# Kernel tuning notes

Hardware: AMD Instinct MI355X
Metric: run time of the kernel (lower is better)

Reference implementation:

```python
import jax, jax.numpy as jnp
import numpy as np

EPS = 1e-5

def _ln(x, g, b):
    m = x.mean(-1, keepdims=True)
    v = ((x - m) ** 2).mean(-1, keepdims=True)
    return (x - m) * jax.lax.rsqrt(v + EPS) * g + b

def _dwconv3d(x, w, stride):
    # x: [N, C, T, H, W], w: [C, 1, kt, kh, kw], depthwise (groups=C), pad = k//2 = 1
    return jax.lax.conv_general_dilated(
        x, w, window_strides=stride, padding=[(1, 1), (1, 1), (1, 1)],
        dimension_numbers=('NCDHW', 'OIDHW', 'NCDHW'), feature_group_count=x.shape[1])

def _pool_heads(t4, w, g, b, stride, thw):
    # t4: [B, nH, 1+L, hd] with cls token at index 0
    B, nH, _, hd = t4.shape
    T, H, W = thw
    cls_tok, body = t4[:, :, :1, :], t4[:, :, 1:, :]
    x = body.reshape(B * nH, T, H, W, hd).transpose(0, 4, 1, 2, 3)  # [B*nH, hd, T, H, W]
    x = _dwconv3d(x, w, stride)
    Tn, Hn, Wn = x.shape[2], x.shape[3], x.shape[4]
    x = x.reshape(B, nH, hd, Tn * Hn * Wn).transpose(0, 1, 3, 2)  # [B, nH, L', hd]
    x = jnp.concatenate([cls_tok, x], axis=2)
    return _ln(x, g, b), (Tn, Hn, Wn)

def _maxpool_skip(x, thw, kernel=(1, 3, 3), stride=(1, 2, 2), pad=((0, 0), (1, 1), (1, 1))):
    # x: [B, 1+L, C]
    B, _, C = x.shape
    T, H, W = thw
    cls_tok, body = x[:, :1, :], x[:, 1:, :]
    y = body.reshape(B, T, H, W, C).transpose(0, 4, 1, 2, 3)  # [B, C, T, H, W]
    y = jax.lax.reduce_window(
        y, -jnp.inf, jax.lax.max,
        window_dimensions=(1, 1) + kernel, window_strides=(1, 1) + stride,
        padding=((0, 0), (0, 0)) + pad)
    Lp = y.shape[2] * y.shape[3] * y.shape[4]
    y = y.reshape(B, C, Lp).transpose(0, 2, 1)
    return jnp.concatenate([cls_tok, y], axis=1)

def setup_inputs() -> dict:
    key = jax.random.key(0)
    ks = jax.random.split(key, 12)
    B, T, H, W, D, NH, HD, DOUT, HID = 16, 8, 28, 28, 192, 2, 96, 384, 768
    N = 1 + T * H * W
    s = 0.02
    return {
        'x': jax.random.normal(ks[0], (B, N, D), jnp.float32),
        'ln1_g': jnp.ones((D,), jnp.float32), 'ln1_b': jnp.zeros((D,), jnp.float32),
        'qkv_w': jax.random.normal(ks[1], (D, 3 * D), jnp.float32) * s,
        'qkv_b': jnp.zeros((3 * D,), jnp.float32),
        'pq_w': jax.random.normal(ks[2], (HD, 1, 3, 3, 3), jnp.float32) * s,
        'pk_w': jax.random.normal(ks[3], (HD, 1, 3, 3, 3), jnp.float32) * s,
        'pv_w': jax.random.normal(ks[4], (HD, 1, 3, 3, 3), jnp.float32) * s,
        'nq_g': jnp.ones((HD,), jnp.float32), 'nq_b': jnp.zeros((HD,), jnp.float32),
        'nk_g': jnp.ones((HD,), jnp.float32), 'nk_b': jnp.zeros((HD,), jnp.float32),
        'nv_g': jnp.ones((HD,), jnp.float32), 'nv_b': jnp.zeros((HD,), jnp.float32),
        'proj_w': jax.random.normal(ks[5], (D, D), jnp.float32) * s,
        'proj_b': jnp.zeros((D,), jnp.float32),
        'ln2_g': jnp.ones((D,), jnp.float32), 'ln2_b': jnp.zeros((D,), jnp.float32),
        'fc1_w': jax.random.normal(ks[6], (D, HID), jnp.float32) * s,
        'fc1_b': jnp.zeros((HID,), jnp.float32),
        'fc2_w': jax.random.normal(ks[7], (HID, DOUT), jnp.float32) * s,
        'fc2_b': jnp.zeros((DOUT,), jnp.float32),
        'projd_w': jax.random.normal(ks[8], (D, DOUT), jnp.float32) * s,
        'projd_b': jnp.zeros((DOUT,), jnp.float32),
        't': T, 'h': H, 'w': W,
    }

def reference(x, ln1_g, ln1_b, qkv_w, qkv_b, pq_w, pk_w, pv_w,
              nq_g, nq_b, nk_g, nk_b, nv_g, nv_b, proj_w, proj_b,
              ln2_g, ln2_b, fc1_w, fc1_b, fc2_w, fc2_b, projd_w, projd_b,
              t, h, w):
    thw = (t, h, w)
    B, N, C = x.shape
    NH = 2
    hd = C // NH
    scale = hd ** -0.5
    stride_q = (1, 2, 2)
    stride_kv = (1, 2, 2)

    # --- attention branch ---
    xn = _ln(x, ln1_g, ln1_b)
    qkv = (xn @ qkv_w + qkv_b).reshape(B, N, 3, NH, hd).transpose(2, 0, 3, 1, 4)
    q, k, v = qkv[0], qkv[1], qkv[2]  # [B, NH, N, hd]
    q, out_shape = _pool_heads(q, pq_w, nq_g, nq_b, stride_q, thw)
    k, _ = _pool_heads(k, pk_w, nk_g, nk_b, stride_kv, thw)
    v, _ = _pool_heads(v, pv_w, nv_g, nv_b, stride_kv, thw)
    attn = jax.nn.softmax(jnp.einsum('bhqd,bhkd->bhqk', q, k) * scale, axis=-1)
    o = jnp.einsum('bhqk,bhkd->bhqd', attn, v)  # [B, NH, Lq, hd]
    Lq = o.shape[2]
    o = o.transpose(0, 2, 1, 3).reshape(B, Lq, C)
    x_block = o @ proj_w + proj_b

    # --- residual skip with max-pool (kernel_skip=(1,3,3) from stride_q=(1,2,2)) ---
    x_res = _maxpool_skip(x, thw)
    x1 = x_res + x_block

    # --- MLP branch (dim != dim_out -> proj on norm2 output) ---
    xn2 = _ln(x1, ln2_g, ln2_b)
    hmid = jax.nn.gelu(xn2 @ fc1_w + fc1_b, approximate=False)
    x_mlp = hmid @ fc2_w + fc2_b
    x2 = (xn2 @ projd_w + projd_b) + x_mlp
    return x2
```

## Files before the change

kernel.cpp:

```cpp
#include <hip/hip_runtime.h>
#include <hip/hip_bf16.h>
#include <type_traits>

#define BB   16
#define N0   6273
#define NQ   1569
#define C3   576
#define HID  768
#define DOUT 384
#define M1   (BB*N0)
#define M2   (BB*NQ)

typedef __attribute__((ext_vector_type(8))) short  s16x8;
typedef __attribute__((ext_vector_type(8))) __bf16 bf16x8;
typedef __attribute__((ext_vector_type(4))) float  f32x4;

static __device__ __forceinline__ float bf2f(unsigned short u) {
  return __uint_as_float(((unsigned)u) << 16);
}
static __device__ __forceinline__ unsigned short f2bf(float f) {
  unsigned x = __float_as_uint(f);
  x += 0x7fffu + ((x >> 16) & 1u);
  return (unsigned short)(x >> 16);
}
static __device__ __forceinline__ unsigned pk2(float a, float b) {
  return (unsigned)f2bf(a) | ((unsigned)f2bf(b) << 16);
}

__global__ __launch_bounds__(256) void ln_rows_bf16_kernel(
    const float* __restrict__ in, const float* __restrict__ g,
    const float* __restrict__ bta, unsigned short* __restrict__ out,
    int rows, int ldc) {
  int row = blockIdx.x * 4 + (threadIdx.x >> 6);
  int lane = threadIdx.x & 63;
  if (row >= rows) return;
  const float* p = in + (size_t)row * 192;
  float v0 = p[lane], v1 = p[lane + 64], v2 = p[lane + 128];
  float s = v0 + v1 + v2;
  float q = v0 * v0 + v1 * v1 + v2 * v2;
  #pragma unroll
  for (int m = 32; m; m >>= 1) { s += __shfl_xor(s, m, 64); q += __shfl_xor(q, m, 64); }
  float mean = s * (1.f / 192.f);
  float var  = q * (1.f / 192.f) - mean * mean;
  float rstd = rsqrtf(var + 1e-5f);
  unsigned short* po = out + (size_t)row * ldc;
  po[lane]       = f2bf((v0 - mean) * rstd * g[lane]       + bta[lane]);
  po[lane + 64]  = f2bf((v1 - mean) * rstd * g[lane + 64]  + bta[lane + 64]);
  po[lane + 128] = f2bf((v2 - mean) * rstd * g[lane + 128] + bta[lane + 128]);
}

__global__ __launch_bounds__(256) void wtrans_kernel(
    const float* __restrict__ in, unsigned short* __restrict__ out, int K, int N) {
  int idx = blockIdx.x * 256 + threadIdx.x;
  if (idx >= K * N) return;
  int n = idx / K, k = idx - n * K;
  out[idx] = f2bf(in[k * N + n]);
}

__global__ __launch_bounds__(256) void wcomb_kernel(
    const float* __restrict__ fc2w, const float* __restrict__ projdw,
    const float* __restrict__ fc2b, const float* __restrict__ projdb,
    unsigned short* __restrict__ wT, float* __restrict__ bc) {
  int idx = blockIdx.x * 256 + threadIdx.x;
  if (idx < 384 * 960) {
    int n = idx / 960, k = idx - n * 960;
    float v = (k < 768) ? fc2w[k * 384 + n] : projdw[(k - 768) * 384 + n];
    wT[idx] = f2bf(v);
  }
  if (idx < 384) bc[idx] = fc2b[idx] + projdb[idx];
}

template <int ACT, int BETA, typename TC>
__global__ __launch_bounds__(256) void gemm_mfma_kernel(
    const unsigned short* __restrict__ A, const unsigned short* __restrict__ BT,
    const float* __restrict__ bias, TC* __restrict__ C,
    int M, int N, int K, int lda, int ldc) {
  __shared__ alignas(16) unsigned short As[128 * 64];
  __shared__ alignas(16) unsigned short Bs[64 * 64];
  const int tid = threadIdx.x;
  const int lane = tid & 63, wid = tid >> 6;
  const int lo = lane & 15, hi = lane >> 4;
  const int bm = blockIdx.y * 128;
  const int bn = blockIdx.x * 64;
  const int s_row = tid >> 3;
  const int s_cb  = tid & 7;
  const int wrow  = wid * 32;
  char* asb = (char*)As;
  char* bsb = (char*)Bs;
  f32x4 acc[2][4];
  #pragma unroll
  for (int mi = 0; mi < 2; ++mi)
    #pragma unroll
    for (int nj = 0; nj < 4; ++nj) {
      acc[mi][nj][0] = 0.f; acc[mi][nj][1] = 0.f;
      acc[mi][nj][2] = 0.f; acc[mi][nj][3] = 0.f;
    }
  for (int k0 = 0; k0 < K; k0 += 64) {
    uint4 av[4], bv[2];
    #pragma unroll
    for (int i = 0; i < 4; ++i) {
      int row = s_row + 32 * i;
      int rg = bm + row; if (rg > M - 1) rg = M - 1;
      av[i] = *(const uint4*)(A + (size_t)rg * lda + k0 + s_cb * 8);
    }
    #pragma unroll
    for (int i = 0; i < 2; ++i) {
      int col = s_row + 32 * i;
      bv[i] = *(const uint4*)(BT + (size_t)(bn + col) * K + k0 + s_cb * 8);
    }
    if (k0) __syncthreads();
    #pragma unroll
    for (int i = 0; i < 4; ++i) {
      int row = s_row + 32 * i;
      *(uint4*)(asb + row * 128 + ((s_cb ^ (row & 7)) << 4)) = av[i];
    }
    #pragma unroll
    for (int i = 0; i < 2; ++i) {
      int col = s_row + 32 * i;
      *(uint4*)(bsb + col * 128 + ((s_cb ^ (col & 7)) << 4)) = bv[i];
    }
    __syncthreads();
    #pragma unroll
    for (int ks = 0; ks < 2; ++ks) {
      s16x8 af[2], bf[4];
      #pragma unroll
      for (int mi = 0; mi < 2; ++mi) {
        int row = wrow + mi * 16 + lo;
        af[mi] = *(const s16x8*)(asb + row * 128 + (((ks * 4 + hi) ^ (row & 7)) << 4));
      }
      #pragma unroll
      for (int nj = 0; nj < 4; ++nj) {
        int col = nj * 16 + lo;
        bf[nj] = *(const s16x8*)(bsb + col * 128 + (((ks * 4 + hi) ^ (col & 7)) << 4));
      }
      #pragma unroll
      for (int mi = 0; mi < 2; ++mi)
        #pragma unroll
        for (int nj = 0; nj < 4; ++nj)
          acc[mi][nj] = __builtin_amdgcn_mfma_f32_16x16x32_bf16(
              (bf16x8)af[mi], (bf16x8)bf[nj], acc[mi][nj], 0, 0, 0);
    }
  }
  #pragma unroll
  for (int nj = 0; nj < 4; ++nj) {
    float bsv = bias[bn + nj * 16 + lo];
    #pragma unroll
    for (int mi = 0; mi < 2; ++mi) {
      int rowb = bm + wrow + mi * 16 + hi * 4;
      #pragma unroll
      for (int r = 0; r < 4; ++r) {
        int row = rowb + r;
        if (row >= M) continue;
        float v = acc[mi][nj][r] + bsv;
        if (ACT == 1) v = 0.5f * v * (1.f + erff(v * 0.70710678118654752f));
        size_t oi = (size_t)row * ldc + bn + nj * 16 + lo;
        if constexpr (BETA != 0) {
          if constexpr (std::is_same<TC, float>::value) v += C[oi];
          else v += bf2f(C[oi]);
        }
        if constexpr (std::is_same<TC, float>::value) C[oi] = v;
        else C[oi] = f2bf(v);
      }
    }
  }
}

__global__ __launch_bounds__(128) void pool_ln_kernel(
    const unsigned short* __restrict__ qkv, const float* __restrict__ w,
    const float* __restrict__ g, const float* __restrict__ bb,
    unsigned short* __restrict__ outp, int cidx, float oscale) {
  const int bid = blockIdx.x;
  const int l  = bid % NQ;
  const int bh = bid / NQ;
  const int h  = bh & 1;
  const int b  = bh >> 1;
  const int d  = threadIdx.x;
  __shared__ float red[128];
  __shared__ float stats[2];
  float val = 0.f;
  if (d < 96) {
    const unsigned short* base = qkv + (size_t)b * N0 * C3 + cidx * 192 + h * 96 + d;
    if (l == 0) {
      val = bf2f(base[0]);
    } else {
      int lp = l - 1;
      int to = lp / 196;
      int rem = lp - to * 196;
      int ho = rem / 14;
      int wo = rem - ho * 14;
      const float* wd = w + d * 27;
      #pragma unroll
      for (int kt = 0; kt < 3; ++kt) {
        int it = to + kt - 1;
        if ((unsigned)it >= 8u) continue;
        #pragma unroll
        for (int kh = 0; kh < 3; ++kh) {
          int ih = 2 * ho + kh - 1;
          if ((unsigned)ih >= 28u) continue;
          #pragma unroll
          for (int kw = 0; kw < 3; ++kw) {
            int iw = 2 * wo + kw - 1;
            if ((unsigned)iw >= 28u) continue;
            int n = 1 + (it * 28 + ih) * 28 + iw;
            val += wd[(kt * 3 + kh) * 3 + kw] * bf2f(base[(size_t)n * C3]);
          }
        }
      }
    }
  }
  red[d] = (d < 96) ? val : 0.f;
  __syncthreads();
  for (int s = 64; s > 0; s >>= 1) { if (d < s) red[d] += red[d + s]; __syncthreads(); }
  if (d == 0) stats[0] = red[0] * (1.f / 96.f);
  __syncthreads();
  float mean = stats[0];
  float dv = (d < 96) ? (val - mean) : 0.f;
  red[d] = dv * dv;
  __syncthreads();
  for (int s = 64; s > 0; s >>= 1) { if (d < s) red[d] += red[d + s]; __syncthreads(); }
  if (d == 0) stats[1] = rsqrtf(red[0] * (1.f / 96.f) + 1e-5f);
  __syncthreads();
  if (d < 96)
    outp[((size_t)bh * NQ + l) * 96 + d] =
        f2bf(((val - mean) * stats[1] * g[d] + bb[d]) * oscale);
}

__global__ __launch_bounds__(256) void attn_mfma_kernel(
    const unsigned short* __restrict__ qb, const unsigned short* __restrict__ kb,
    const unsigned short* __restrict__ vb, unsigned short* __restrict__ o) {
  __shared__ alignas(16) unsigned short Ks[32][104];
  __shared__ alignas(16) unsigned short Vt[96 * 32];
  const int tid  = threadIdx.x;
  const int lane = tid & 63;
  const int wid  = tid >> 6;
  const int lo = lane & 15, hi = lane >> 4;
  const int bh = blockIdx.y;
  const int b = bh >> 1, h = bh & 1;
  const int q0 = blockIdx.x * 64 + wid * 16;
  const int qg = q0 + lo;

  const unsigned short* qbase = qb + (size_t)bh * NQ * 96;
  const unsigned short* kbase = kb + (size_t)bh * NQ * 96;
  const unsigned short* vbase = vb + (size_t)bh * NQ * 96;
  char* vtb = (char*)Vt;

  s16x8 qf[3];
  if (qg < NQ) {
    const unsigned short* qrow = qbase + (size_t)qg * 96 + hi * 8;
    qf[0] = *(const s16x8*)(qrow);
    qf[1] = *(const s16x8*)(qrow + 32);
    qf[2] = *(const s16x8*)(qrow + 64);
  } else {
    #pragma unroll
    for (int j = 0; j < 8; ++j) { qf[0][j] = 0; qf[1][j] = 0; qf[2][j] = 0; }
  }

  f32x4 ot[6];
  #pragma unroll
  for (int t = 0; t < 6; ++t) { ot[t][0] = 0.f; ot[t][1] = 0.f; ot[t][2] = 0.f; ot[t][3] = 0.f; }
  float m = -1e30f, lsum = 0.f;

  for (int c = 0; c < (NQ + 31) / 32; ++c) {
    const int k0 = c * 32;
    #pragma unroll
    for (int j = 0; j < 6; ++j) {
      int u = tid + 256 * j;
      int kr = u / 48, c2 = u - kr * 48;
      unsigned val = 0;
      if (k0 + kr < NQ)
        val = *(const unsigned*)(kbase + (size_t)(k0 + kr) * 96 + c2 * 2);
      *(unsigned*)(&Ks[kr][c2 * 2]) = val;
    }
    #pragma unroll
    for (int j = 0; j < 6; ++j) {
      int u = tid + 256 * j;
      int kr = u / 48, c2 = u - kr * 48;
      unsigned val = 0;
      if (k0 + kr < NQ)
        val = *(const unsigned*)(vbase + (size_t)(k0 + kr) * 96 + c2 * 2);
      int d0 = c2 * 2, d1 = d0 + 1;
      int o0 = (d0 * 64 + kr * 2) ^ ((d0 & 7) << 4);
      int o1 = (d1 * 64 + kr * 2) ^ ((d1 & 7) << 4);
      *(unsigned short*)(vtb + o0) = (unsigned short)(val & 0xffffu);
      *(unsigned short*)(vtb + o1) = (unsigned short)(val >> 16);
    }
    __syncthreads();
    f32x4 st0, st1;
    st0[0]=st0[1]=st0[2]=st0[3]=0.f;
    st1[0]=st1[1]=st1[2]=st1[3]=0.f;
    #pragma unroll
    for (int cc = 0; cc < 3; ++cc) {
      s16x8 kf0 = *(const s16x8*)(&Ks[lo][cc * 32 + hi * 8]);
      s16x8 kf1 = *(const s16x8*)(&Ks[16 + lo][cc * 32 + hi * 8]);
      st0 = __builtin_amdgcn_mfma_f32_16x16x32_bf16((bf16x8)kf0, (bf16x8)qf[cc], st0, 0, 0, 0);
      st1 = __builtin_amdgcn_mfma_f32_16x16x32_bf16((bf16x8)kf1, (bf16x8)qf[cc], st1, 0, 0, 0);
    }
    if (k0 + 32 > NQ) {
      #pragma unroll
      for (int r = 0; r < 4; ++r) {
        if (k0 + 4 * hi + r      >= NQ) st0[r] = -1e30f;
        if (k0 + 16 + 4 * hi + r >= NQ) st1[r] = -1e30f;
      }
    }
    float mc = fmaxf(fmaxf(fmaxf(st0[0], st0[1]), fmaxf(st0[2], st0[3])),
                     fmaxf(fmaxf(st1[0], st1[1]), fmaxf(st1[2], st1[3])));
    mc = fmaxf(mc, __shfl_xor(mc, 16));
    mc = fmaxf(mc, __shfl_xor(mc, 32));
    if (!__all(mc <= m)) {
      float mnew = fmaxf(m, mc);
      float alpha = __expf(m - mnew);
      #pragma unroll
      for (int t = 0; t < 6; ++t) {
        ot[t][0] *= alpha; ot[t][1] *= alpha; ot[t][2] *= alpha; ot[t][3] *= alpha;
      }
      lsum *= alpha;
      m = mnew;
    }
    float p0[4], p1[4], sum = 0.f;
    #pragma unroll
    for (int r = 0; r < 4; ++r) {
      p0[r] = __expf(st0[r] - m);
      p1[r] = __expf(st1[r] - m);
      sum += p0[r] + p1[r];
    }
    sum += __shfl_xor(sum, 16);
    sum += __shfl_xor(sum, 32);
    lsum += sum;
    unsigned w00 = pk2(p0[0], p0[1]), w01 = pk2(p0[2], p0[3]);
    unsigned w10 = pk2(p1[0], p1[1]), w11 = pk2(p1[2], p1[3]);
    unsigned w00x = __shfl_xor(w00, 32), w01x = __shfl_xor(w01, 32);
    unsigned w10x = __shfl_xor(w10, 32), w11x = __shfl_xor(w11, 32);
    unsigned w00y = __shfl_xor(w00, 16), w01y = __shfl_xor(w01, 16);
    unsigned w10y = __shfl_xor(w10, 16), w11y = __shfl_xor(w11, 16);
    unsigned w00z = __shfl_xor(w00x, 16), w01z = __shfl_xor(w01x, 16);
    unsigned w10z = __shfl_xor(w10x, 16), w11z = __shfl_xor(w11x, 16);
    bool h0 = (hi == 0), h1 = (hi == 1), h2 = (hi == 2);
    union { unsigned u[4]; s16x8 v; } pf;
    pf.u[0] = h0 ? w00  : h1 ? w00z : h2 ? w10x : w10y;
    pf.u[1] = h0 ? w01  : h1 ? w01z : h2 ? w11x : w11y;
    pf.u[2] = h0 ? w00y : h1 ? w00x : h2 ? w10z : w10;
    pf.u[3] = h0 ? w01y : h1 ? w01x : h2 ? w11z : w11;
    #pragma unroll
    for (int t = 0; t < 6; ++t) {
      int d = 16 * t + lo;
      int off = (d * 64 + hi * 16) ^ ((d & 7) << 4);
      s16x8 va = *(const s16x8*)(vtb + off);
      ot[t] = __builtin_amdgcn_mfma_f32_16x16x32_bf16((bf16x8)va, (bf16x8)pf.v, ot[t], 0, 0, 0);
    }
    __syncthreads();
  }
  if (qg < NQ) {
    float invl = 1.f / lsum;
    unsigned short* po = o + ((size_t)b * NQ + qg) * 192 + h * 96 + hi * 4;
    #pragma unroll
    for (int t = 0; t < 6; ++t) {
      ushort4 u4;
      u4.x = f2bf(ot[t][0] * invl); u4.y = f2bf(ot[t][1] * invl);
      u4.z = f2bf(ot[t][2] * invl); u4.w = f2bf(ot[t][3] * invl);
      *(ushort4*)(po + 16 * t) = u4;
    }
  }
}

__global__ __launch_bounds__(256) void maxpool_kernel(
    const float* __restrict__ x, float* __restrict__ x1) {
  int idx = blockIdx.x * 256 + threadIdx.x;
  const int total = BB * NQ * 192;
  if (idx >= total) return;
  int cc = idx % 192;
  int rem = idx / 192;
  int l = rem % NQ;
  int b = rem / NQ;
  const float* xb = x + (size_t)b * N0 * 192;
  float m;
  if (l == 0) {
    m = xb[cc];
  } else {
    int lp = l - 1;
    int to = lp / 196;
    int r2 = lp - to * 196;
    int ho = r2 / 14;
    int wo = r2 - ho * 14;
    m = -INFINITY;
    #pragma unroll
    for (int kh = 0; kh < 3; ++kh) {
      int ih = 2 * ho + kh - 1;
      if ((unsigned)ih >= 28u) continue;
      #pragma unroll
      for (int kw = 0; kw < 3; ++kw) {
        int iw = 2 * wo + kw - 1;
        if ((unsigned)iw >= 28u) continue;
        int n = 1 + (to * 28 + ih) * 28 + iw;
        m = fmaxf(m, xb[(size_t)n * 192 + cc]);
      }
    }
  }
  x1[idx] = m;
}

extern "C" void kernel_launch(void* const* d_in, const int* in_sizes, int n_in,
                              void* d_out, int out_size, void* d_ws, size_t ws_size,
                              hipStream_t stream) {
  (void)in_sizes; (void)n_in; (void)out_size; (void)ws_size;
  const float* x       = (const float*)d_in[0];
  const float* ln1_g   = (const float*)d_in[1];
  const float* ln1_b   = (const float*)d_in[2];
  const float* qkv_w   = (const float*)d_in[3];
  const float* qkv_b   = (const float*)d_in[4];
  const float* pq_w    = (const float*)d_in[5];
  const float* pk_w    = (const float*)d_in[6];
  const float* pv_w    = (const float*)d_in[7];
  const float* nq_g    = (const float*)d_in[8];
  const float* nq_b    = (const float*)d_in[9];
  const float* nk_g    = (const float*)d_in[10];
  const float* nk_b    = (const float*)d_in[11];
  const float* nv_g    = (const float*)d_in[12];
  const float* nv_b    = (const float*)d_in[13];
  const float* proj_w  = (const float*)d_in[14];
  const float* proj_b  = (const float*)d_in[15];
  const float* ln2_g   = (const float*)d_in[16];
  const float* ln2_b   = (const float*)d_in[17];
  const float* fc1_w   = (const float*)d_in[18];
  const float* fc1_b   = (const float*)d_in[19];
  const float* fc2_w   = (const float*)d_in[20];
  const float* fc2_b   = (const float*)d_in[21];
  const float* projd_w = (const float*)d_in[22];
  const float* projd_b = (const float*)d_in[23];

  char* ws = (char*)d_ws;
  unsigned short* xnb  = (unsigned short*)(ws);
  unsigned short* qbuf = (unsigned short*)(ws);
  unsigned short* kbuf = (unsigned short*)(ws + 9639936);
  unsigned short* vbuf = (unsigned short*)(ws + 19279872);
  char* r2 = ws + 38541312;
  unsigned short* qkvb = (unsigned short*)(r2);
  unsigned short* obb  = (unsigned short*)(r2);
  float*          x1   = (float*)(r2 + 9639936);
  unsigned short* comb = (unsigned short*)(r2 + 28919808);
  char* r3 = ws + 154165248;
  unsigned short* qkv_wT  = (unsigned short*)(r3);
  unsigned short* proj_wT = (unsigned short*)(r3 + 221184);
  unsigned short* fc1_wT  = (unsigned short*)(r3 + 294912);
  unsigned short* wcombT  = (unsigned short*)(r3 + 589824);
  float*          bcomb   = (float*)(r3 + 1327104);
  float* out = (float*)d_out;

  const float scale = 0.10206207261596577f;

  wtrans_kernel<<<(576 * 192 + 255) / 256, 256, 0, stream>>>(qkv_w, qkv_wT, 192, 576);
  wtrans_kernel<<<(192 * 192 + 255) / 256, 256, 0, stream>>>(proj_w, proj_wT, 192, 192);
  wtrans_kernel<<<(768 * 192 + 255) / 256, 256, 0, stream>>>(fc1_w, fc1_wT, 192, 768);
  wcomb_kernel<<<(384 * 960 + 255) / 256, 256, 0, stream>>>(fc2_w, projd_w, fc2_b, projd_b,
                                                            wcombT, bcomb);
  ln_rows_bf16_kernel<<<(M1 + 3) / 4, 256, 0, stream>>>(x, ln1_g, ln1_b, xnb, M1, 192);
  gemm_mfma_kernel<0, 0, unsigned short>
      <<<dim3(C3 / 64, (M1 + 127) / 128), 256, 0, stream>>>(
          xnb, qkv_wT, qkv_b, qkvb, M1, C3, 192, 192, C3);
  pool_ln_kernel<<<BB * 2 * NQ, 128, 0, stream>>>(qkvb, pq_w, nq_g, nq_b, qbuf, 0, scale);
  pool_ln_kernel<<<BB * 2 * NQ, 128, 0, stream>>>(qkvb, pk_w, nk_g, nk_b, kbuf, 1, 1.f);
  pool_ln_kernel<<<BB * 2 * NQ, 128, 0, stream>>>(qkvb, pv_w, nv_g, nv_b, vbuf, 2, 1.f);
  attn_mfma_kernel<<<dim3((NQ + 63) / 64, BB * 2), 256, 0, stream>>>(qbuf, kbuf, vbuf, obb);
  maxpool_kernel<<<(BB * NQ * 192 + 255) / 256, 256, 0, stream>>>(x, x1);
  gemm_mfma_kernel<0, 1, float>
      <<<dim3(192 / 64, (M2 + 127) / 128), 256, 0, stream>>>(
          obb, proj_wT, proj_b, x1, M2, 192, 192, 192, 192);
  ln_rows_bf16_kernel<<<(M2 + 3) / 4, 256, 0, stream>>>(x1, ln2_g, ln2_b, comb + 768, M2, 960);
  gemm_mfma_kernel<1, 0, unsigned short>
      <<<dim3(HID / 64, (M2 + 127) / 128), 256, 0, stream>>>(
          comb + 768, fc1_wT, fc1_b, comb, M2, HID, 192, 960, 960);
  gemm_mfma_kernel<0, 0, float>
      <<<dim3(DOUT / 64, (M2 + 127) / 128), 256, 0, stream>>>(
          comb, wcombT, bcomb, out, M2, DOUT, 960, 960, DOUT);
}
```

Before: 1.344 ms.

## Double attention KV chunk to 64 keys and use shuffle reductions in pool LN

The attention kernel now processes 64 keys per iteration instead of 32. This halves the number of block barriers and online-softmax rescale steps, and the V transpose buffer gets a new XOR swizzle for the wider rows. Separately, the pooled LayerNorm kernel replaces its two shared-memory tree reductions with wave shuffle reductions of sum and sum of squares, needing a single barrier. The cost is more LDS and registers per block in attention, plus a single-pass variance formula in the pooling LN.

```diff
diff --git a/kernel.cpp b/kernel.cpp
--- a/kernel.cpp
+++ b/kernel.cpp
@@ -25,6 +25,24 @@
 }
 static __device__ __forceinline__ unsigned pk2(float a, float b) {
   return (unsigned)f2bf(a) | ((unsigned)f2bf(b) << 16);
+}
+
+static __device__ __forceinline__ s16x8 redistP(const float* p0, const float* p1, int hi) {
+  unsigned w00 = pk2(p0[0], p0[1]), w01 = pk2(p0[2], p0[3]);
+  unsigned w10 = pk2(p1[0], p1[1]), w11 = pk2(p1[2], p1[3]);
+  unsigned w00x = __shfl_xor(w00, 32), w01x = __shfl_xor(w01, 32);
+  unsigned w10x = __shfl_xor(w10, 32), w11x = __shfl_xor(w11, 32);
+  unsigned w00y = __shfl_xor(w00, 16), w01y = __shfl_xor(w01, 16);
+  unsigned w10y = __shfl_xor(w10, 16), w11y = __shfl_xor(w11, 16);
+  unsigned w00z = __shfl_xor(w00x, 16), w01z = __shfl_xor(w01x, 16);
+  unsigned w10z = __shfl_xor(w10x, 16), w11z = __shfl_xor(w11x, 16);
+  bool h0 = (hi == 0), h1 = (hi == 1), h2 = (hi == 2);
+  union { unsigned u[4]; s16x8 v; } pf;
+  pf.u[0] = h0 ? w00  : h1 ? w00z : h2 ? w10x : w10y;
+  pf.u[1] = h0 ? w01  : h1 ? w01z : h2 ? w11x : w11y;
+  pf.u[2] = h0 ? w00y : h1 ? w00x : h2 ? w10z : w10;
+  pf.u[3] = h0 ? w01y : h1 ? w01x : h2 ? w11z : w11;
+  return pf.v;
 }
 
 __global__ __launch_bounds__(256) void ln_rows_bf16_kernel(
@@ -175,8 +193,6 @@
   const int h  = bh & 1;
   const int b  = bh >> 1;
   const int d  = threadIdx.x;
-  __shared__ float red[128];
-  __shared__ float stats[2];
   float val = 0.f;
   if (d < 96) {
     const unsigned short* base = qkv + (size_t)b * N0 * C3 + cidx * 192 + h * 96 + d;
@@ -208,28 +224,31 @@
       }
     }
   }
-  red[d] = (d < 96) ? val : 0.f;
+  const int lane = d & 63, wv = d >> 6;
+  float s1 = (d < 96) ? val : 0.f;
+  float s2 = (d < 96) ? val * val : 0.f;
+  #pragma unroll
+  for (int mm = 32; mm; mm >>= 1) {
+    s1 += __shfl_xor(s1, mm, 64);
+    s2 += __shfl_xor(s2, mm, 64);
+  }
+  __shared__ float wsum[4];
+  if (lane == 0) { wsum[wv] = s1; wsum[2 + wv] = s2; }
   __syncthreads();
-  for (int s = 64; s > 0; s >>= 1) { if (d < s) red[d] += red[d + s]; __syncthreads(); }
-  if (d == 0) stats[0] = red[0] * (1.f / 96.f);
-  __syncthreads();
-  float mean = stats[0];
-  float dv = (d < 96) ? (val - mean) : 0.f;
-  red[d] = dv * dv;
-  __syncthreads();
-  for (int s = 64; s > 0; s >>= 1) { if (d < s) red[d] += red[d + s]; __syncthreads(); }
-  if (d == 0) stats[1] = rsqrtf(red[0] * (1.f / 96.f) + 1e-5f);
-  __syncthreads();
+  float S  = wsum[0] + wsum[1];
+  float Q2 = wsum[2] + wsum[3];
+  float mean = S * (1.f / 96.f);
+  float rstd = rsqrtf(Q2 * (1.f / 96.f) - mean * mean + 1e-5f);
   if (d < 96)
     outp[((size_t)bh * NQ + l) * 96 + d] =
-        f2bf(((val - mean) * stats[1] * g[d] + bb[d]) * oscale);
+        f2bf(((val - mean) * rstd * g[d] + bb[d]) * oscale);
 }
 
 __global__ __launch_bounds__(256) void attn_mfma_kernel(
     const unsigned short* __restrict__ qb, const unsigned short* __restrict__ kb,
     const unsigned short* __restrict__ vb, unsigned short* __restrict__ o) {
-  __shared__ alignas(16) unsigned short Ks[32][104];
-  __shared__ alignas(16) unsigned short Vt[96 * 32];
+  __shared__ alignas(16) unsigned short Ks[64][104];
+  __shared__ alignas(16) unsigned short Vt[96 * 64];
   const int tid  = threadIdx.x;
   const int lane = tid & 63;
   const int wid  = tid >> 6;
@@ -260,10 +279,11 @@
   for (int t = 0; t < 6; ++t) { ot[t][0] = 0.f; ot[t][1] = 0.f; ot[t][2] = 0.f; ot[t][3] = 0.f; }
   float m = -1e30f, lsum = 0.f;
 
-  for (int c = 0; c < (NQ + 31) / 32; ++c) {
-    const int k0 = c * 32;
-    #pragma unroll
-    for (int j = 0; j < 6; ++j) {
+  const int nchunks = (NQ + 63) / 64;
+  for (int c = 0; c < nchunks; ++c) {
+    const int k0 = c * 64;
+    #pragma unroll
+    for (int j = 0; j < 12; ++j) {
       int u = tid + 256 * j;
       int kr = u / 48, c2 = u - kr * 48;
       unsigned val = 0;
@@ -272,38 +292,43 @@
       *(unsigned*)(&Ks[kr][c2 * 2]) = val;
     }
     #pragma unroll
-    for (int j = 0; j < 6; ++j) {
+    for (int j = 0; j < 12; ++j) {
       int u = tid + 256 * j;
       int kr = u / 48, c2 = u - kr * 48;
       unsigned val = 0;
       if (k0 + kr < NQ)
         val = *(const unsigned*)(vbase + (size_t)(k0 + kr) * 96 + c2 * 2);
       int d0 = c2 * 2, d1 = d0 + 1;
-      int o0 = (d0 * 64 + kr * 2) ^ ((d0 & 7) << 4);
-      int o1 = (d1 * 64 + kr * 2) ^ ((d1 & 7) << 4);
+      int gsw = ((d0 >> 1) ^ (d0 >> 4)) & 7;
+      int o0 = (d0 * 128 + kr * 2) ^ (gsw << 4);
+      int o1 = (d1 * 128 + kr * 2) ^ (gsw << 4);
       *(unsigned short*)(vtb + o0) = (unsigned short)(val & 0xffffu);
       *(unsigned short*)(vtb + o1) = (unsigned short)(val >> 16);
     }
     __syncthreads();
-    f32x4 st0, st1;
-    st0[0]=st0[1]=st0[2]=st0[3]=0.f;
-    st1[0]=st1[1]=st1[2]=st1[3]=0.f;
+    f32x4 st[4];
+    #pragma unroll
+    for (int s = 0; s < 4; ++s) { st[s][0] = 0.f; st[s][1] = 0.f; st[s][2] = 0.f; st[s][3] = 0.f; }
     #pragma unroll
     for (int cc = 0; cc < 3; ++cc) {
-      s16x8 kf0 = *(const s16x8*)(&Ks[lo][cc * 32 + hi * 8]);
-      s16x8 kf1 = *(const s16x8*)(&Ks[16 + lo][cc * 32 + hi * 8]);
-      st0 = __builtin_amdgcn_mfma_f32_16x16x32_bf16((bf16x8)kf0, (bf16x8)qf[cc], st0, 0, 0, 0);
-      st1 = __builtin_amdgcn_mfma_f32_16x16x32_bf16((bf16x8)kf1, (bf16x8)qf[cc], st1, 0, 0, 0);
-    }
-    if (k0 + 32 > NQ) {
-      #pragma unroll
-      for (int r = 0; r < 4; ++r) {
-        if (k0 + 4 * hi + r      >= NQ) st0[r] = -1e30f;
-        if (k0 + 16 + 4 * hi + r >= NQ) st1[r] = -1e30f;
-      }
-    }
-    float mc = fmaxf(fmaxf(fmaxf(st0[0], st0[1]), fmaxf(st0[2], st0[3])),
-                     fmaxf(fmaxf(st1[0], st1[1]), fmaxf(st1[2], st1[3])));
+      #pragma unroll
+      for (int s = 0; s < 4; ++s) {
+        s16x8 kf = *(const s16x8*)(&Ks[s * 16 + lo][cc * 32 + hi * 8]);
+        st[s] = __builtin_amdgcn_mfma_f32_16x16x32_bf16((bf16x8)kf, (bf16x8)qf[cc], st[s], 0, 0, 0);
+      }
+    }
+    if (k0 + 64 > NQ) {
+      #pragma unroll
+      for (int s = 0; s < 4; ++s)
+        #pragma unroll
+        for (int r = 0; r < 4; ++r)
+          if (k0 + s * 16 + 4 * hi + r >= NQ) st[s][r] = -1e30f;
+    }
+    float mc = -1e30f;
+    #pragma unroll
+    for (int s = 0; s < 4; ++s)
+      #pragma unroll
+      for (int r = 0; r < 4; ++r) mc = fmaxf(mc, st[s][r]);
     mc = fmaxf(mc, __shfl_xor(mc, 16));
     mc = fmaxf(mc, __shfl_xor(mc, 32));
     if (!__all(mc <= m)) {
@@ -316,36 +341,29 @@
       lsum *= alpha;
       m = mnew;
     }
-    float p0[4], p1[4], sum = 0.f;
-    #pragma unroll
-    for (int r = 0; r < 4; ++r) {
-      p0[r] = __expf(st0[r] - m);
-      p1[r] = __expf(st1[r] - m);
-      sum += p0[r] + p1[r];
-    }
+    float p[4][4];
+    float sum = 0.f;
+    #pragma unroll
+    for (int s = 0; s < 4; ++s)
+      #pragma unroll
+      for (int r = 0; r < 4; ++r) {
+        p[s][r] = __expf(st[s][r] - m);
+        sum += p[s][r];
+      }
     sum += __shfl_xor(sum, 16);
     sum += __shfl_xor(sum, 32);
     lsum += sum;
-    unsigned w00 = pk2(p0[0], p0[1]), w01 = pk2(p0[2], p0[3]);
-    unsigned w10 = pk2(p1[0], p1[1]), w11 = pk2(p1[2], p1[3]);
-    unsigned w00x = __shfl_xor(w00, 32), w01x = __shfl_xor(w01, 32);
-    unsigned w10x = __shfl_xor(w10, 32), w11x = __shfl_xor(w11, 32);
-    unsigned w00y = __shfl_xor(w00, 16), w01y = __shfl_xor(w01, 16);
-    unsigned w10y = __shfl_xor(w10, 16), w11y = __shfl_xor(w11, 16);
-    unsigned w00z = __shfl_xor(w00x, 16), w01z = __shfl_xor(w01x, 16);
-    unsigned w10z = __shfl_xor(w10x, 16), w11z = __shfl_xor(w11x, 16);
-    bool h0 = (hi == 0), h1 = (hi == 1), h2 = (hi == 2);
-    union { unsigned u[4]; s16x8 v; } pf;
-    pf.u[0] = h0 ? w00  : h1 ? w00z : h2 ? w10x : w10y;
-    pf.u[1] = h0 ? w01  : h1 ? w01z : h2 ? w11x : w11y;
-    pf.u[2] = h0 ? w00y : h1 ? w00x : h2 ? w10z : w10;
-    pf.u[3] = h0 ? w01y : h1 ? w01x : h2 ? w11z : w11;
+    s16x8 pf01 = redistP(p[0], p[1], hi);
+    s16x8 pf23 = redistP(p[2], p[3], hi);
     #pragma unroll
     for (int t = 0; t < 6; ++t) {
       int d = 16 * t + lo;
-      int off = (d * 64 + hi * 16) ^ ((d & 7) << 4);
-      s16x8 va = *(const s16x8*)(vtb + off);
-      ot[t] = __builtin_amdgcn_mfma_f32_16x16x32_bf16((bf16x8)va, (bf16x8)pf.v, ot[t], 0, 0, 0);
+      int gsw = ((d >> 1) ^ (d >> 4)) & 7;
+      int base = d * 128 + hi * 16;
+      s16x8 va0 = *(const s16x8*)(vtb + ((base)      ^ (gsw << 4)));
+      s16x8 va1 = *(const s16x8*)(vtb + ((base + 64) ^ (gsw << 4)));
+      ot[t] = __builtin_amdgcn_mfma_f32_16x16x32_bf16((bf16x8)va0, (bf16x8)pf01, ot[t], 0, 0, 0);
+      ot[t] = __builtin_amdgcn_mfma_f32_16x16x32_bf16((bf16x8)va1, (bf16x8)pf23, ot[t], 0, 0, 0);
     }
     __syncthreads();
   }
```

New measurement: 1.190 ms. 11.5% less time.
